# Kernel optimization log

Measured on AMD Instinct MI355X. Metric: run time of the kernel, lower is better.

Reference implementation:

```python
import jax, jax.numpy as jnp
import numpy as np

N_LEVELS = 16
N_FEATURES = 2
MIN_RES = 16
MAX_RES = 512
HASH_SIZE = 19
TABLE_SIZE = 2 ** HASH_SIZE
# per-level grid resolutions (geometric progression, matches torch buffer)
RESOLUTIONS = [int(MIN_RES * (MAX_RES / MIN_RES) ** (i / (N_LEVELS - 1))) for i in range(N_LEVELS)]
# 8 cube-corner offsets, [8, 3] (same ordering as torch.meshgrid indexing='ij')
OFFSETS = np.stack(np.meshgrid(np.array([0, 1]), np.array([0, 1]), np.array([0, 1]), indexing='ij')).reshape(3, -1).T.astype(np.int64)
PRIMES = np.array([1, 2654435761, 805459861], dtype=np.int64)


def setup_inputs() -> dict:
    key = jax.random.key(0)
    k1, k2 = jax.random.split(key)
    N = 1 << 20  # ~1M sample points (e.g., 4096 rays x 256 samples)
    x = jax.random.uniform(k1, (N, 3), dtype=jnp.float32, minval=-1.0, maxval=1.0)
    tables = jax.random.uniform(k2, (N_LEVELS, TABLE_SIZE, N_FEATURES), dtype=jnp.float32, minval=-1e-4, maxval=1e-4)
    return {"x": x, "tables": tables}


def reference(x, tables):
    x = jnp.clip(x.astype(jnp.float32), -1.0, 1.0)  # [N, 3]
    offsets = jnp.asarray(OFFSETS)                  # [8, 3] int64
    primes = jnp.asarray(PRIMES)                    # [3] int64
    outs = []
    for i, res in enumerate(RESOLUTIONS):
        coords = x * res                            # [N, 3]
        cf = jnp.floor(coords)
        lc = coords - cf                            # fractional part, [N, 3]
        # 8 corner integer coords, wrapped into [0, res): [N, 8, 3]
        corners = (cf.astype(jnp.int64)[:, None, :] + offsets[None]) % res
        corners_f = corners.astype(jnp.float32) / res
        # spatial hash: quantize to [0, 2^18) grid then prime-multiply hash
        q = ((corners_f + 1.0) * 0.5 * (2.0 ** 18)).astype(jnp.int64)
        hashed = (q * primes).sum(-1) % TABLE_SIZE  # [N, 8]
        feats = tables[i][hashed]                   # gather, [N, 8, F]
        # trilinear weights: prod over dims of (1-lc) if offset==0 else lc
        w = jnp.where(offsets[None] == 0, 1.0 - lc[:, None, :], lc[:, None, :]).prod(-1)  # [N, 8]
        outs.append((w[..., None] * feats).sum(1))  # [N, F]
    return jnp.concatenate(outs, axis=-1)           # [N, L*F]
```

## Files before the change

kernel.cpp:

```cpp
#include <hip/hip_runtime.h>


static constexpr int      kNLevels   = 16;
static constexpr unsigned kTableSize = 1u << 19;
static constexpr unsigned kMask      = kTableSize - 1u;
static constexpr unsigned kP1        = 2654435761u;
static constexpr unsigned kP2        = 805459861u;

typedef float v4f __attribute__((ext_vector_type(4)));
typedef float v2f __attribute__((ext_vector_type(2)));

constexpr int RES_[kNLevels]  = {16, 20, 25, 32, 40, 50, 64, 80,
                                 101, 127, 161, 203, 256, 322, 406, 512};
constexpr int QOFF_[kNLevels] = {0, 16, 36, 61, 93, 133, 183, 247,
                                 327, 428, 555, 716, 919, 1175, 1497, 1903};
static constexpr int kQTot = 2415;

constexpr unsigned qval_rcp(int c, int res) {
    const float r = 1.0f / (float)res;
    const float v = (float)c * r;
    const float s = ((v + 1.0f) * 0.5f) * 262144.0f;
    return (unsigned)s;
}

struct QTab {
    unsigned v[kQTot];
    constexpr QTab() : v{} {
        int o = 0;
        for (int i = 0; i < kNLevels; ++i) {
            for (int c = 0; c < RES_[i]; ++c) v[o + c] = qval_rcp(c, RES_[i]);
            o += RES_[i];
        }
    }
};
__constant__ QTab QT = QTab();

__device__ __forceinline__ void level_idx_w(
    const int i, const unsigned* __restrict__ sq,
    const float px, const float py, const float pz,
    unsigned* __restrict__ idx, float* __restrict__ w)
{
    const int   res  = RES_[i];
    const float resf = (float)res;
    const unsigned* qt = sq + QOFF_[i];

    const float cxf = px * resf, cyf = py * resf, czf = pz * resf;
    const float fx = floorf(cxf), fy = floorf(cyf), fz = floorf(czf);
    const float lx = cxf - fx, ly = cyf - fy, lz = czf - fz;

    const int ix = (int)fx, iy = (int)fy, iz = (int)fz;
    const int cx0 = ix < 0 ? ix + res : (ix >= res ? ix - res : ix);
    const int cy0 = iy < 0 ? iy + res : (iy >= res ? iy - res : iy);
    const int cz0 = iz < 0 ? iz + res : (iz >= res ? iz - res : iz);
    const int cx1 = (cx0 + 1 == res) ? 0 : cx0 + 1;
    const int cy1 = (cy0 + 1 == res) ? 0 : cy0 + 1;
    const int cz1 = (cz0 + 1 == res) ? 0 : cz0 + 1;

    const unsigned qx0 = qt[cx0], qx1 = qt[cx1];
    const unsigned qy0 = qt[cy0], qy1 = qt[cy1];
    const unsigned qz0 = qt[cz0], qz1 = qt[cz1];

    const unsigned hy0 = qy0 * kP1, hy1 = qy1 * kP1;
    const unsigned hz0 = qz0 * kP2, hz1 = qz1 * kP2;

    const float wx0 = 1.0f - lx, wx1 = lx;
    const float wy0 = 1.0f - ly, wy1 = ly;
    const float wz0 = 1.0f - lz, wz1 = lz;

#pragma unroll
    for (int m = 0; m < 8; ++m) {
        const unsigned h = ((m & 4) ? qx1 : qx0) +
                           ((m & 2) ? hy1 : hy0) +
                           ((m & 1) ? hz1 : hz0);
        idx[m] = h & kMask;
        w[m] = (((m & 4) ? wx1 : wx0) * ((m & 2) ? wy1 : wy0)) *
               ((m & 1) ? wz1 : wz0);
    }
}

__global__ __launch_bounds__(256, 6) void hashenc_kernel(
    const float* __restrict__ x,
    const float* __restrict__ tables,
    float* __restrict__ out,
    int N)
{
    __shared__ unsigned sq[kQTot];
    for (int t = threadIdx.x; t < kQTot; t += 256) sq[t] = QT.v[t];
    __syncthreads();

    const int n = blockIdx.x * 256 + threadIdx.x;
    if (n >= N) return;

    float px = x[3 * n + 0];
    float py = x[3 * n + 1];
    float pz = x[3 * n + 2];
    px = fminf(fmaxf(px, -1.0f), 1.0f);
    py = fminf(fmaxf(py, -1.0f), 1.0f);
    pz = fminf(fmaxf(pz, -1.0f), 1.0f);

    v4f* op = (v4f*)(out + (size_t)n * (2 * kNLevels));

#pragma unroll
    for (int ip = 0; ip < kNLevels / 2; ++ip) {
        const int iA = 2 * ip, iB = 2 * ip + 1;

        unsigned ia[8], ib[8];
        float    wa[8], wb[8];
        level_idx_w(iA, sq, px, py, pz, ia, wa);
        level_idx_w(iB, sq, px, py, pz, ib, wb);

        const v2f* tA = (const v2f*)tables + (size_t)iA * kTableSize;
        const v2f* tB = (const v2f*)tables + (size_t)iB * kTableSize;

        v2f fa[8], fb[8];
#pragma unroll
        for (int m = 0; m < 8; ++m) fa[m] = tA[ia[m]];
#pragma unroll
        for (int m = 0; m < 8; ++m) fb[m] = tB[ib[m]];

        float a0 = 0.0f, a1 = 0.0f, b0 = 0.0f, b1 = 0.0f;
#pragma unroll
        for (int m = 0; m < 8; ++m) {
            a0 += wa[m] * fa[m].x;
            a1 += wa[m] * fa[m].y;
        }
#pragma unroll
        for (int m = 0; m < 8; ++m) {
            b0 += wb[m] * fb[m].x;
            b1 += wb[m] * fb[m].y;
        }

        v4f v = {a0, a1, b0, b1};
        op[ip] = v;
    }
}

extern "C" void kernel_launch(void* const* d_in, const int* in_sizes, int n_in,
                              void* d_out, int out_size, void* d_ws, size_t ws_size,
                              hipStream_t stream) {
    const float* x      = (const float*)d_in[0];
    const float* tables = (const float*)d_in[1];
    float*       out    = (float*)d_out;
    const int N = in_sizes[0] / 3;
    const int blocks = (N + 255) / 256;
    hipLaunchKernelGGL(hashenc_kernel, dim3(blocks), dim3(256), 0, stream,
                       x, tables, out, N);
}
```

Before: 1.022 ms.

## Bin points by Morton cell and encode in spatially sorted order

Adds a counting sort of input points into 32^3 Morton-ordered bins (zero, histogram, single-block scan, atomic scatter) that builds a permutation. The encoder then processes points in this order, with a block-index swizzle, so neighbouring threads hit nearby hash-table entries and cache locality improves for the random gathers. The cost is four extra kernel launches, global atomics, and scattered reads of x and writes of out through the permutation. It also leaves an unused stub function. The sorted path only runs when the workspace is large enough.

```diff
diff --git a/kernel.cpp b/kernel.cpp
--- a/kernel.cpp
+++ b/kernel.cpp
@@ -6,6 +6,8 @@
 static constexpr unsigned kMask      = kTableSize - 1u;
 static constexpr unsigned kP1        = 2654435761u;
 static constexpr unsigned kP2        = 805459861u;
+
+static constexpr int kNBins = 32768;
 
 typedef float v4f __attribute__((ext_vector_type(4)));
 typedef float v2f __attribute__((ext_vector_type(2)));
@@ -78,18 +80,96 @@
     }
 }
 
-__global__ __launch_bounds__(256, 6) void hashenc_kernel(
+__device__ __forceinline__ void encode_point(
+    const unsigned* __restrict__ sq, const float* __restrict__ tables,
+    float* __restrict__ out, const int n)
+{
+    float px = out ? 0.0f : 0.0f;
+    (void)px;
+}
+
+__device__ __forceinline__ unsigned spread5(unsigned x) {
+    x &= 0x3ffu;
+    x = (x | (x << 16)) & 0x30000FFu;
+    x = (x | (x << 8))  & 0x300F00Fu;
+    x = (x | (x << 4))  & 0x30C30C3u;
+    x = (x | (x << 2))  & 0x9249249u;
+    return x;
+}
+
+__device__ __forceinline__ unsigned point_bin(const float* __restrict__ x, int n) {
+    float px = fminf(fmaxf(x[3 * n + 0], -1.0f), 1.0f);
+    float py = fminf(fmaxf(x[3 * n + 1], -1.0f), 1.0f);
+    float pz = fminf(fmaxf(x[3 * n + 2], -1.0f), 1.0f);
+    int cx = (int)((px + 1.0f) * 16.0f); cx = cx > 31 ? 31 : cx;
+    int cy = (int)((py + 1.0f) * 16.0f); cy = cy > 31 ? 31 : cy;
+    int cz = (int)((pz + 1.0f) * 16.0f); cz = cz > 31 ? 31 : cz;
+    return spread5((unsigned)cx) | (spread5((unsigned)cy) << 1) |
+           (spread5((unsigned)cz) << 2);
+}
+
+__global__ void zero_kernel(unsigned* __restrict__ p, int n) {
+    int i = blockIdx.x * 256 + threadIdx.x;
+    if (i < n) p[i] = 0u;
+}
+
+__global__ void hist_kernel(const float* __restrict__ x,
+                            unsigned* __restrict__ counts, int N) {
+    int n = blockIdx.x * 256 + threadIdx.x;
+    if (n >= N) return;
+    atomicAdd(&counts[point_bin(x, n)], 1u);
+}
+
+__global__ __launch_bounds__(1024) void scan_kernel(
+    const unsigned* __restrict__ counts, unsigned* __restrict__ cursor) {
+    __shared__ unsigned sh[1024];
+    const int t = threadIdx.x;
+    unsigned loc[32];
+    unsigned s = 0;
+#pragma unroll
+    for (int j = 0; j < 32; ++j) { loc[j] = s; s += counts[t * 32 + j]; }
+    sh[t] = s;
+    __syncthreads();
+    for (int off = 1; off < 1024; off <<= 1) {
+        unsigned v = (t >= off) ? sh[t - off] : 0u;
+        __syncthreads();
+        sh[t] += v;
+        __syncthreads();
+    }
+    const unsigned base = sh[t] - s;
+#pragma unroll
+    for (int j = 0; j < 32; ++j) cursor[t * 32 + j] = base + loc[j];
+}
+
+__global__ void scatter_kernel(const float* __restrict__ x,
+                               unsigned* __restrict__ cursor,
+                               unsigned* __restrict__ perm, int N) {
+    int n = blockIdx.x * 256 + threadIdx.x;
+    if (n >= N) return;
+    unsigned pos = atomicAdd(&cursor[point_bin(x, n)], 1u);
+    perm[pos] = (unsigned)n;
+}
+
+template <bool SORTED>
+__global__ __launch_bounds__(256, 6) void hashenc_kernel_t(
     const float* __restrict__ x,
     const float* __restrict__ tables,
     float* __restrict__ out,
+    const unsigned* __restrict__ perm,
     int N)
 {
     __shared__ unsigned sq[kQTot];
     for (int t = threadIdx.x; t < kQTot; t += 256) sq[t] = QT.v[t];
     __syncthreads();
 
-    const int n = blockIdx.x * 256 + threadIdx.x;
-    if (n >= N) return;
+    int bid = blockIdx.x;
+    if (SORTED) {
+        const int nblk = gridDim.x;
+        if ((nblk & 7) == 0) bid = (bid & 7) * (nblk >> 3) + (bid >> 3);
+    }
+    const int g = bid * 256 + threadIdx.x;
+    if (g >= N) return;
+    const int n = SORTED ? (int)perm[g] : g;
 
     float px = x[3 * n + 0];
     float py = x[3 * n + 1];
@@ -142,7 +222,26 @@
     const float* tables = (const float*)d_in[1];
     float*       out    = (float*)d_out;
     const int N = in_sizes[0] / 3;
-    const int blocks = (N + 255) / 256;
-    hipLaunchKernelGGL(hashenc_kernel, dim3(blocks), dim3(256), 0, stream,
-                       x, tables, out, N);
-}
+    const int pb = (N + 255) / 256;
+
+    const size_t need = ((size_t)2 * kNBins + (size_t)N) * sizeof(unsigned);
+    if (d_ws != nullptr && ws_size >= need) {
+        unsigned* counts = (unsigned*)d_ws;
+        unsigned* cursor = counts + kNBins;
+        unsigned* perm   = cursor + kNBins;
+
+        hipLaunchKernelGGL(zero_kernel, dim3((kNBins + 255) / 256), dim3(256),
+                           0, stream, counts, kNBins);
+        hipLaunchKernelGGL(hist_kernel, dim3(pb), dim3(256), 0, stream,
+                           x, counts, N);
+        hipLaunchKernelGGL(scan_kernel, dim3(1), dim3(1024), 0, stream,
+                           counts, cursor);
+        hipLaunchKernelGGL(scatter_kernel, dim3(pb), dim3(256), 0, stream,
+                           x, cursor, perm, N);
+        hipLaunchKernelGGL((hashenc_kernel_t<true>), dim3(pb), dim3(256),
+                           0, stream, x, tables, out, perm, N);
+    } else {
+        hipLaunchKernelGGL((hashenc_kernel_t<false>), dim3(pb), dim3(256),
+                           0, stream, x, tables, out, nullptr, N);
+    }
+}
```

New measurement: 991.1 us. 1.03x faster.
